# Performance work log

Hardware: AMD Instinct MI355X
Metric: run time of the kernel (lower is better)

The kernel has to match this reference:

```python
import jax, jax.numpy as jnp
import numpy as np
import math

ALPHA = 2.0   # ATan surrogate default alpha
TAU = 2.0     # LIF tau
VTH = 1.0     # v_threshold default
EPS = 1e-5    # BatchNorm eps
T, N, C, H, W = 16, 32, 128, 32, 32
COUT = 128

@jax.custom_vjp
def atan_spike(x):
    return (x >= 0).astype(x.dtype)

def _spike_fwd(x):
    return (x >= 0).astype(x.dtype), x

def _spike_bwd(x, g):
    return (g * (ALPHA / 2) / (1.0 + (math.pi / 2 * ALPHA * x) ** 2),)

atan_spike.defvjp(_spike_fwd, _spike_bwd)

def lif_scan(x):
    # MultiStepLIFNode, decay_input=False, v_reset=0.0, detach_reset=True:
    #   v <- v + (x_t - (v - 0)) / tau ; spike = H(v - vth) ; v <- v * (1 - sg(spike))
    def step(v, x_t):
        v = v + (x_t - v) / TAU
        s = atan_spike(v - VTH)
        v = v * (1.0 - jax.lax.stop_gradient(s))
        return v, s
    v0 = jnp.zeros_like(x[0])
    _, spikes = jax.lax.scan(step, v0, x)
    return spikes  # [T, N, C, H, W]

def setup_inputs() -> dict:
    key = jax.random.key(0)
    ks = jax.random.split(key, 9)
    x = jax.random.normal(ks[0], (T, N, C, H, W), dtype=jnp.float32)
    dw_w = jax.random.normal(ks[1], (C, 1, 3, 3), dtype=jnp.float32) * (1.0 / 3.0)
    dw_b = jax.random.normal(ks[2], (C,), dtype=jnp.float32) * 0.01
    pw_w = jax.random.normal(ks[3], (COUT, C), dtype=jnp.float32) * (1.0 / math.sqrt(C))
    pw_b = jax.random.normal(ks[4], (COUT,), dtype=jnp.float32) * 0.01
    gamma = jnp.ones((COUT,), dtype=jnp.float32)
    beta = jnp.zeros((COUT,), dtype=jnp.float32)
    run_mean = jax.random.normal(ks[5], (COUT,), dtype=jnp.float32) * 0.1
    run_var = jax.random.uniform(ks[6], (COUT,), dtype=jnp.float32) + 0.5
    return {"x": x, "dw_w": dw_w, "dw_b": dw_b, "pw_w": pw_w, "pw_b": pw_b,
            "gamma": gamma, "beta": beta, "run_mean": run_mean, "run_var": run_var}

def reference(x, dw_w, dw_b, pw_w, pw_b, gamma, beta, run_mean, run_var):
    s = lif_scan(x)                          # [T,N,C,H,W] spikes
    s2 = s.reshape(T * N, C, H, W)           # seq_to_ann_forward flattening
    # depthwise 3x3, stride 1, pad 1
    y = jax.lax.conv_general_dilated(
        s2, dw_w, window_strides=(1, 1), padding="SAME",
        feature_group_count=C,
        dimension_numbers=("NCHW", "OIHW", "NCHW"))
    y = y + dw_b[None, :, None, None]
    # pointwise 1x1
    y = jnp.einsum("nchw,oc->nohw", y, pw_w) + pw_b[None, :, None, None]
    # BatchNorm2d (inference mode, running stats)
    scale = gamma / jnp.sqrt(run_var + EPS)
    y = (y - run_mean[None, :, None, None]) * scale[None, :, None, None] + beta[None, :, None, None]
    return y.reshape(T, N, COUT, H, W)
```

## Files before the change

### kernel.cpp

```cpp
#include <hip/hip_runtime.h>
#include <hip/hip_bf16.h>
#include <stdint.h>

#define T_    16
#define N_    32
#define C_    128
#define HW_   1024
#define COUT_ 128

typedef __bf16 bf16x8 __attribute__((ext_vector_type(8)));
typedef float  f32x4  __attribute__((ext_vector_type(4)));

__global__ __launch_bounds__(256) void k0_prep(
    const float* __restrict__ pw_w, const float* __restrict__ pw_b,
    const float* __restrict__ gamma, const float* __restrict__ beta,
    const float* __restrict__ mean,  const float* __restrict__ var,
    __bf16* __restrict__ wbf, float* __restrict__ scale2, float* __restrict__ bias2) {
  int idx = blockIdx.x * 256 + threadIdx.x;
  if (idx < COUT_ * C_) wbf[idx] = (__bf16)pw_w[idx];
  if (idx < COUT_) {
    float s = gamma[idx] * rsqrtf(var[idx] + 1e-5f);
    scale2[idx] = s;
    bias2[idx]  = beta[idx] + (pw_b[idx] - mean[idx]) * s;
  }
}

__global__ __launch_bounds__(256) void k1_lif(const float* __restrict__ x,
                                              uint32_t* __restrict__ S) {
  int nc   = blockIdx.x;
  int tid  = threadIdx.x;
  int lane = tid & 63;
  int w    = tid >> 6;
  size_t base = (size_t)nc * HW_;
  unsigned long long* S64 = (unsigned long long*)S;

  float v0 = 0.f, v1 = 0.f, v2 = 0.f, v3 = 0.f;
#pragma unroll
  for (int t = 0; t < T_; ++t) {
    const float* xp = x + (size_t)t * (N_ * C_ * HW_) + base;
    float x0 = xp[tid];
    float x1 = xp[256 + tid];
    float x2 = xp[512 + tid];
    float x3 = xp[768 + tid];
    v0 = v0 + (x0 - v0) * 0.5f; bool s0 = (v0 >= 1.0f); if (s0) v0 = 0.f;
    v1 = v1 + (x1 - v1) * 0.5f; bool s1 = (v1 >= 1.0f); if (s1) v1 = 0.f;
    v2 = v2 + (x2 - v2) * 0.5f; bool s2 = (v2 >= 1.0f); if (s2) v2 = 0.f;
    v3 = v3 + (x3 - v3) * 0.5f; bool s3 = (v3 >= 1.0f); if (s3) v3 = 0.f;
    unsigned long long m0 = __ballot(s0);
    unsigned long long m1 = __ballot(s1);
    unsigned long long m2 = __ballot(s2);
    unsigned long long m3 = __ballot(s3);
    if (lane == 0) {
      size_t b64 = ((size_t)nc * T_ + t) * 16;
      S64[b64 + 0  + w] = m0;
      S64[b64 + 4  + w] = m1;
      S64[b64 + 8  + w] = m2;
      S64[b64 + 12 + w] = m3;
    }
  }
}

__global__ __launch_bounds__(256) void k2_main(
    const uint32_t* __restrict__ S,
    const float* __restrict__ dww, const float* __restrict__ dwb,
    const __bf16* __restrict__ wbf,
    const float* __restrict__ scale2, const float* __restrict__ bias2,
    float* __restrict__ out) {
  __shared__ uint32_t sb[C_ * 8];
  __shared__ __bf16  Blds[128 * 136];

  const int bid   = blockIdx.x;
  const int n_img = bid >> 3;
  const int rg    = bid & 7;
  const int t_img = n_img >> 5;
  const int n_in  = n_img & 31;
  const int r0    = rg * 4;
  const int tid   = threadIdx.x;

#pragma unroll
  for (int k = 0; k < 3; ++k) {
    int li = k * 256 + tid;
    int c  = li / 6;
    int ri = li - c * 6;
    int gr = r0 - 1 + ri;
    uint32_t wv = 0;
    if (gr >= 0 && gr < 32)
      wv = S[(((size_t)n_in * C_ + c) * T_ + t_img) * 32 + gr];
    sb[c * 8 + ri] = wv;
  }
  __syncthreads();

  {
    int c    = tid & 127;
    int half = tid >> 7;
    float w9[9];
#pragma unroll
    for (int i = 0; i < 9; ++i) w9[i] = dww[c * 9 + i];
    float bias = dwb[c];
    uint64_t R[6];
#pragma unroll
    for (int q = 0; q < 6; ++q) R[q] = ((uint64_t)sb[c * 8 + q]) << 1;

    int col0 = half * 16;
#pragma unroll 4
    for (int ci = 0; ci < 16; ++ci) {
      int col = col0 + ci;
      float acc[4] = {bias, bias, bias, bias};
#pragma unroll
      for (int q = 0; q < 6; ++q) {
        uint32_t tri = (uint32_t)(R[q] >> col) & 7u;
        float b0 = (float)(tri & 1u);
        float b1 = (float)((tri >> 1) & 1u);
        float b2 = (float)(tri >> 2);
#pragma unroll
        for (int kh = 0; kh < 3; ++kh) {
          int r = q - kh;
          if (r >= 0 && r < 4) {
            acc[r] += w9[kh * 3 + 0] * b0;
            acc[r] += w9[kh * 3 + 1] * b1;
            acc[r] += w9[kh * 3 + 2] * b2;
          }
        }
      }
#pragma unroll
      for (int r = 0; r < 4; ++r)
        Blds[(r * 32 + col) * 136 + c] = (__bf16)acc[r];
    }
  }
  __syncthreads();

  const int lane  = tid & 63;
  const int wid   = tid >> 6;
  const int ohalf = wid >> 1;
  const int hhalf = wid & 1;
  const int m16   = lane & 15;
  const int q4    = lane >> 4;

  f32x4 acc[4][4];
#pragma unroll
  for (int mt = 0; mt < 4; ++mt)
#pragma unroll
    for (int nt = 0; nt < 4; ++nt)
      acc[mt][nt] = (f32x4){0.f, 0.f, 0.f, 0.f};

#pragma unroll
  for (int ks = 0; ks < 4; ++ks) {
    const int k0 = ks * 32 + q4 * 8;
    bf16x8 af[4], bfr[4];
#pragma unroll
    for (int mt = 0; mt < 4; ++mt) {
      int m = ohalf * 64 + mt * 16 + m16;
      af[mt] = *(const bf16x8*)(wbf + m * 128 + k0);
    }
#pragma unroll
    for (int nt = 0; nt < 4; ++nt) {
      int hw = hhalf * 64 + nt * 16 + m16;
      bfr[nt] = *(const bf16x8*)(Blds + hw * 136 + k0);
    }
#pragma unroll
    for (int nt = 0; nt < 4; ++nt)
#pragma unroll
      for (int mt = 0; mt < 4; ++mt)
        acc[mt][nt] = __builtin_amdgcn_mfma_f32_16x16x32_bf16(af[mt], bfr[nt], acc[mt][nt], 0, 0, 0);
  }

#pragma unroll
  for (int mt = 0; mt < 4; ++mt) {
    int ob = ohalf * 64 + mt * 16 + q4 * 4;
    f32x4 sc = *(const f32x4*)(scale2 + ob);
    f32x4 bs = *(const f32x4*)(bias2 + ob);
#pragma unroll
    for (int nt = 0; nt < 4; ++nt) {
      int hw = hhalf * 64 + nt * 16 + m16;
      size_t obase = (size_t)n_img * (COUT_ * HW_) + (size_t)rg * 128 + hw;
#pragma unroll
      for (int ri = 0; ri < 4; ++ri) {
        out[obase + (size_t)(ob + ri) * HW_] = acc[mt][nt][ri] * sc[ri] + bs[ri];
      }
    }
  }
}

extern "C" void kernel_launch(void* const* d_in, const int* in_sizes, int n_in_args,
                              void* d_out, int out_size, void* d_ws, size_t ws_size,
                              hipStream_t stream) {
  const float* x     = (const float*)d_in[0];
  const float* dw_w  = (const float*)d_in[1];
  const float* dw_b  = (const float*)d_in[2];
  const float* pw_w  = (const float*)d_in[3];
  const float* pw_b  = (const float*)d_in[4];
  const float* gamma = (const float*)d_in[5];
  const float* beta  = (const float*)d_in[6];
  const float* rmean = (const float*)d_in[7];
  const float* rvar  = (const float*)d_in[8];
  float* out = (float*)d_out;

  uint32_t* S    = (uint32_t*)d_ws;
  __bf16* wbf    = (__bf16*)((char*)d_ws + (size_t)N_ * C_ * T_ * 128);
  float* scale2  = (float*)((char*)wbf + (size_t)COUT_ * C_ * 2);
  float* bias2   = scale2 + COUT_;

  k0_prep<<<64, 256, 0, stream>>>(pw_w, pw_b, gamma, beta, rmean, rvar, wbf, scale2, bias2);
  k1_lif<<<N_ * C_, 256, 0, stream>>>(x, S);
  k2_main<<<(T_ * N_) * 8, 256, 0, stream>>>(S, dw_w, dw_b, wbf, scale2, bias2, out);
}
```

Before: 495.5 us.

## Vectorize LIF loads and stage GEMM output through LDS for coalesced stores

The LIF kernel now loads four consecutive floats per thread as one vector and re-interleaves the four ballot masks with bit tricks so the spike bitmask layout stays the same. The main kernel swaps the MFMA operand roles so each lane holds four consecutive spatial positions per output channel. Results are then staged through shared memory (aliased onto the B buffer) in two halves and written back as contiguous 16-byte stores per row. This targets poorly coalesced scalar global stores of the dominant output tensor and scalar input loads, at the cost of extra syncs and LDS traffic.

```diff
diff --git a/kernel.cpp b/kernel.cpp
--- a/kernel.cpp
+++ b/kernel.cpp
@@ -27,35 +27,37 @@
 
 __global__ __launch_bounds__(256) void k1_lif(const float* __restrict__ x,
                                               uint32_t* __restrict__ S) {
-  int nc   = blockIdx.x;
-  int tid  = threadIdx.x;
-  int lane = tid & 63;
-  int w    = tid >> 6;
-  size_t base = (size_t)nc * HW_;
-  unsigned long long* S64 = (unsigned long long*)S;
-
-  float v0 = 0.f, v1 = 0.f, v2 = 0.f, v3 = 0.f;
+  const int nc   = blockIdx.x;
+  const int tid  = threadIdx.x;
+  const int lane = tid & 63;
+  const int wv   = tid >> 6;
+  const size_t base = (size_t)nc * HW_ + 4 * tid;
+
+  f32x4 v = {0.f, 0.f, 0.f, 0.f};
 #pragma unroll
   for (int t = 0; t < T_; ++t) {
-    const float* xp = x + (size_t)t * (N_ * C_ * HW_) + base;
-    float x0 = xp[tid];
-    float x1 = xp[256 + tid];
-    float x2 = xp[512 + tid];
-    float x3 = xp[768 + tid];
-    v0 = v0 + (x0 - v0) * 0.5f; bool s0 = (v0 >= 1.0f); if (s0) v0 = 0.f;
-    v1 = v1 + (x1 - v1) * 0.5f; bool s1 = (v1 >= 1.0f); if (s1) v1 = 0.f;
-    v2 = v2 + (x2 - v2) * 0.5f; bool s2 = (v2 >= 1.0f); if (s2) v2 = 0.f;
-    v3 = v3 + (x3 - v3) * 0.5f; bool s3 = (v3 >= 1.0f); if (s3) v3 = 0.f;
+    const f32x4 xv = *(const f32x4*)(x + (size_t)t * (N_ * C_ * HW_) + base);
+    v = v + (xv - v) * 0.5f;
+    bool s0 = (v.x >= 1.0f); if (s0) v.x = 0.f;
+    bool s1 = (v.y >= 1.0f); if (s1) v.y = 0.f;
+    bool s2 = (v.z >= 1.0f); if (s2) v.z = 0.f;
+    bool s3 = (v.w >= 1.0f); if (s3) v.w = 0.f;
     unsigned long long m0 = __ballot(s0);
     unsigned long long m1 = __ballot(s1);
     unsigned long long m2 = __ballot(s2);
     unsigned long long m3 = __ballot(s3);
-    if (lane == 0) {
-      size_t b64 = ((size_t)nc * T_ + t) * 16;
-      S64[b64 + 0  + w] = m0;
-      S64[b64 + 4  + w] = m1;
-      S64[b64 + 8  + w] = m2;
-      S64[b64 + 12 + w] = m3;
+    if (lane < 8) {
+      uint32_t wrd = 0;
+      unsigned long long mm[4] = {m0, m1, m2, m3};
+#pragma unroll
+      for (int b = 0; b < 4; ++b) {
+        uint32_t by = (uint32_t)(mm[b] >> (lane * 8)) & 0xFFu;
+        by = (by | (by << 12)) & 0x000F000Fu;
+        by = (by | (by << 6))  & 0x03030303u;
+        by = (by | (by << 3))  & 0x11111111u;
+        wrd |= by << b;
+      }
+      S[((size_t)nc * T_ + t) * 32 + wv * 8 + lane] = wrd;
     }
   }
 }
@@ -66,8 +68,10 @@
     const __bf16* __restrict__ wbf,
     const float* __restrict__ scale2, const float* __restrict__ bias2,
     float* __restrict__ out) {
+  __shared__ __align__(16) unsigned char smem_u[34816];
   __shared__ uint32_t sb[C_ * 8];
-  __shared__ __bf16  Blds[128 * 136];
+  __bf16* Blds  = (__bf16*)smem_u;
+  float*  stage = (float*)smem_u;
 
   const int bid   = blockIdx.x;
   const int n_img = bid >> 3;
@@ -83,10 +87,10 @@
     int c  = li / 6;
     int ri = li - c * 6;
     int gr = r0 - 1 + ri;
-    uint32_t wv = 0;
+    uint32_t wvv = 0;
     if (gr >= 0 && gr < 32)
-      wv = S[(((size_t)n_in * C_ + c) * T_ + t_img) * 32 + gr];
-    sb[c * 8 + ri] = wv;
+      wvv = S[(((size_t)n_in * C_ + c) * T_ + t_img) * 32 + gr];
+    sb[c * 8 + ri] = wvv;
   }
   __syncthreads();
 
@@ -136,6 +140,14 @@
   const int m16   = lane & 15;
   const int q4    = lane >> 4;
 
+  float sc_r[4], bs_r[4];
+#pragma unroll
+  for (int nt = 0; nt < 4; ++nt) {
+    int o = ohalf * 64 + nt * 16 + m16;
+    sc_r[nt] = scale2[o];
+    bs_r[nt] = bias2[o];
+  }
+
   f32x4 acc[4][4];
 #pragma unroll
   for (int mt = 0; mt < 4; ++mt)
@@ -146,37 +158,48 @@
 #pragma unroll
   for (int ks = 0; ks < 4; ++ks) {
     const int k0 = ks * 32 + q4 * 8;
-    bf16x8 af[4], bfr[4];
+    bf16x8 hwf[4], of[4];
 #pragma unroll
     for (int mt = 0; mt < 4; ++mt) {
-      int m = ohalf * 64 + mt * 16 + m16;
-      af[mt] = *(const bf16x8*)(wbf + m * 128 + k0);
+      int hw = hhalf * 64 + mt * 16 + m16;
+      hwf[mt] = *(const bf16x8*)(Blds + hw * 136 + k0);
     }
 #pragma unroll
     for (int nt = 0; nt < 4; ++nt) {
-      int hw = hhalf * 64 + nt * 16 + m16;
-      bfr[nt] = *(const bf16x8*)(Blds + hw * 136 + k0);
+      int o = ohalf * 64 + nt * 16 + m16;
+      of[nt] = *(const bf16x8*)(wbf + o * 128 + k0);
     }
 #pragma unroll
     for (int nt = 0; nt < 4; ++nt)
 #pragma unroll
       for (int mt = 0; mt < 4; ++mt)
-        acc[mt][nt] = __builtin_amdgcn_mfma_f32_16x16x32_bf16(af[mt], bfr[nt], acc[mt][nt], 0, 0, 0);
-  }
-
-#pragma unroll
-  for (int mt = 0; mt < 4; ++mt) {
-    int ob = ohalf * 64 + mt * 16 + q4 * 4;
-    f32x4 sc = *(const f32x4*)(scale2 + ob);
-    f32x4 bs = *(const f32x4*)(bias2 + ob);
-#pragma unroll
-    for (int nt = 0; nt < 4; ++nt) {
-      int hw = hhalf * 64 + nt * 16 + m16;
-      size_t obase = (size_t)n_img * (COUT_ * HW_) + (size_t)rg * 128 + hw;
-#pragma unroll
-      for (int ri = 0; ri < 4; ++ri) {
-        out[obase + (size_t)(ob + ri) * HW_] = acc[mt][nt][ri] * sc[ri] + bs[ri];
+        acc[mt][nt] = __builtin_amdgcn_mfma_f32_16x16x32_bf16(hwf[mt], of[nt], acc[mt][nt], 0, 0, 0);
+  }
+
+  const size_t out_img = (size_t)n_img * (COUT_ * HW_) + (size_t)rg * 128;
+#pragma unroll
+  for (int h = 0; h < 2; ++h) {
+    __syncthreads();
+    if (ohalf == h) {
+#pragma unroll
+      for (int nt = 0; nt < 4; ++nt) {
+        int olocal = nt * 16 + m16;
+#pragma unroll
+        for (int mt = 0; mt < 4; ++mt) {
+          int hwl = hhalf * 64 + mt * 16 + q4 * 4;
+          f32x4 vv = acc[mt][nt] * sc_r[nt] + bs_r[nt];
+          *(f32x4*)(stage + olocal * 132 + hwl) = vv;
+        }
       }
+    }
+    __syncthreads();
+#pragma unroll
+    for (int i = 0; i < 8; ++i) {
+      int idx    = i * 256 + tid;
+      int olocal = idx >> 5;
+      int col    = idx & 31;
+      f32x4 vv = *(const f32x4*)(stage + olocal * 132 + col * 4);
+      *(f32x4*)(out + out_img + (size_t)(h * 64 + olocal) * HW_ + col * 4) = vv;
     }
   }
 }
```

Result: no change. 500.1 us (+0.9%).
